# Kernel tuning notes

Hardware: AMD Instinct MI355X
Metric: run time of the kernel (lower is better)

## Reference

```python
import jax, jax.numpy as jnp
import numpy as np

BETA = 0.25
NUM_CODES = 512      # K
CODE_DIM = 64        # D (codebook_size)
N_TOKENS = 131072    # N


def setup_inputs() -> dict:
    key = jax.random.key(0)
    kx, kc = jax.random.split(key)
    x = jax.random.normal(kx, (N_TOKENS, CODE_DIM), dtype=jnp.float32)
    # keras 'random_uniform' initializer: U(-0.05, 0.05)
    codebook = jax.random.uniform(kc, (NUM_CODES, CODE_DIM), dtype=jnp.float32,
                                  minval=-0.05, maxval=0.05)
    return {"x": x, "codebook": codebook}


def reference(x, codebook):
    # Squared Euclidean distances [N, K] via expansion; argmin is identical
    # to argmin of tf.norm (sqrt is monotone).
    x2 = jnp.sum(x * x, axis=-1, keepdims=True)            # [N, 1]
    c2 = jnp.sum(codebook * codebook, axis=-1)             # [K]
    d2 = x2 - 2.0 * (x @ codebook.T) + c2[None, :]         # [N, K]
    indices = jnp.argmin(d2, axis=-1)                      # [N]
    quantized = jnp.take(codebook, indices, axis=0)        # [N, D]

    commitment_loss = jnp.mean((jax.lax.stop_gradient(quantized) - x) ** 2)
    codebook_loss = jnp.mean((quantized - jax.lax.stop_gradient(x)) ** 2)
    loss = BETA * commitment_loss + codebook_loss

    # straight-through estimator
    quantized_st = x + jax.lax.stop_gradient(quantized - x)
    return quantized_st, loss
```

## Files before the change

kernel.cpp:

```cpp
#include <hip/hip_runtime.h>

#define N_TOK 131072
#define K_CODES 512
#define DIM 64
#define MARGIN_S 1e-4f
#define LIST_CAP 30000

typedef __attribute__((ext_vector_type(8))) short bfx8;
typedef __attribute__((ext_vector_type(4))) float f32x4;
typedef __attribute__((ext_vector_type(4))) int i32x4;

__device__ __forceinline__ unsigned short f2bf_rn(float f) {
    unsigned u = __float_as_uint(f);
    unsigned r = (u + 0x7FFF + ((u >> 16) & 1)) >> 16;
    return (unsigned short)r;
}
__device__ __forceinline__ float bf2f(unsigned short h) {
    return __uint_as_float(((unsigned)h) << 16);
}

__device__ __forceinline__ float np_sumsq64(const float* v) {
    float r[8];
#pragma unroll
    for (int j = 0; j < 8; ++j) r[j] = __fmul_rn(v[j], v[j]);
#pragma unroll
    for (int i = 8; i < 64; i += 8) {
#pragma unroll
        for (int j = 0; j < 8; ++j)
            r[j] = __fadd_rn(r[j], __fmul_rn(v[i + j], v[i + j]));
    }
    return __fadd_rn(__fadd_rn(__fadd_rn(r[0], r[1]), __fadd_rn(r[2], r[3])),
                     __fadd_rn(__fadd_rn(r[4], r[5]), __fadd_rn(r[6], r[7])));
}

__global__ __launch_bounds__(256) void vq_prep(
    const float* __restrict__ cb, float* __restrict__ cnorm,
    float* __restrict__ c2h, unsigned short* __restrict__ cbh,
    unsigned short* __restrict__ cbl)
{
    int k = blockIdx.x * 256 + threadIdx.x;
    if (k >= K_CODES) return;
    float v[DIM];
#pragma unroll
    for (int d = 0; d < DIM; ++d) {
        float f = cb[k * DIM + d];
        v[d] = f;
        unsigned short h = f2bf_rn(f);
        cbh[k * DIM + d] = h;
        cbl[k * DIM + d] = f2bf_rn(__fsub_rn(f, bf2f(h)));
    }
    float c2 = np_sumsq64(v);
    cnorm[k] = c2;
    c2h[k] = __fmul_rn(0.5f, c2);
}

__global__ __attribute__((amdgpu_flat_work_group_size(256, 256),
                          amdgpu_waves_per_eu(2, 2)))
void vq_screen(
    const float* __restrict__ x, const float* __restrict__ cb,
    const unsigned short* __restrict__ cbh, const unsigned short* __restrict__ cbl,
    const float* __restrict__ c2h, float* __restrict__ out,
    double* __restrict__ loss_acc, int* __restrict__ counter,
    int* __restrict__ list, int cap)
{
    __shared__ bfx8 lds_h[128 * 8];
    __shared__ bfx8 lds_l[128 * 8];
    __shared__ float lds_c2[K_CODES];
    __shared__ double wsum[4];

    const int tid = threadIdx.x;
    const int wave = (blockIdx.x << 2) + (tid >> 6);
    const int lane = tid & 63;
    const int tokb = wave << 6;
    const int lrow = lane & 15;
    const int lgrp = lane >> 4;
    const int lcol = lrow;

    const float inf = __int_as_float(0x7f800000);

    if (tid < 128) ((float4*)lds_c2)[tid] = ((const float4*)c2h)[tid];

#define SPL(F, J, AH, AL) { unsigned short h_ = f2bf_rn(F); \
    (AH)[J] = (short)h_; (AL)[J] = (short)f2bf_rn(__fsub_rn(F, bf2f(h_))); }
#define LOADX(m) \
    bfx8 ah0_##m, al0_##m, ah1_##m, al1_##m; \
    { const float* xr = x + ((size_t)(tokb + (m) * 16 + lrow) << 6) + (lgrp << 3); \
      float4 f0 = *(const float4*)xr; \
      float4 f1 = *(const float4*)(xr + 4); \
      float4 f2 = *(const float4*)(xr + 32); \
      float4 f3 = *(const float4*)(xr + 36); \
      SPL(f0.x, 0, ah0_##m, al0_##m) SPL(f0.y, 1, ah0_##m, al0_##m) \
      SPL(f0.z, 2, ah0_##m, al0_##m) SPL(f0.w, 3, ah0_##m, al0_##m) \
      SPL(f1.x, 4, ah0_##m, al0_##m) SPL(f1.y, 5, ah0_##m, al0_##m) \
      SPL(f1.z, 6, ah0_##m, al0_##m) SPL(f1.w, 7, ah0_##m, al0_##m) \
      SPL(f2.x, 0, ah1_##m, al1_##m) SPL(f2.y, 1, ah1_##m, al1_##m) \
      SPL(f2.z, 2, ah1_##m, al1_##m) SPL(f2.w, 3, ah1_##m, al1_##m) \
      SPL(f3.x, 4, ah1_##m, al1_##m) SPL(f3.y, 5, ah1_##m, al1_##m) \
      SPL(f3.z, 6, ah1_##m, al1_##m) SPL(f3.w, 7, ah1_##m, al1_##m) }
    LOADX(0) LOADX(1) LOADX(2) LOADX(3)
#undef LOADX
#undef SPL

    f32x4 best0 = {inf, inf, inf, inf}, best1 = best0, best2 = best0, best3 = best0;
    f32x4 sec0 = best0, sec1 = best0, sec2 = best0, sec3 = best0;
    i32x4 idx0 = {0, 0, 0, 0}, idx1 = idx0, idx2 = idx0, idx3 = idx0;

    for (int ph = 0; ph < 4; ++ph) {
        __syncthreads();
        {
            const bfx8* gh = (const bfx8*)cbh + (ph << 10);
            const bfx8* gl = (const bfx8*)cbl + (ph << 10);
#pragma unroll
            for (int it = 0; it < 4; ++it) {
                int g = (it << 8) + tid;
                int code = g >> 3, slot = g & 7;
                int dst = (code << 3) + (slot ^ (code & 7));
                lds_h[dst] = gh[g];
                lds_l[dst] = gl[g];
            }
        }
        __syncthreads();

        int lr_c = lrow;
        int s0_c = lgrp ^ (lr_c & 7);
        bfx8 bh0 = lds_h[(lr_c << 3) + s0_c];
        bfx8 bh1 = lds_h[(lr_c << 3) + (s0_c ^ 4)];
        bfx8 bl0 = lds_l[(lr_c << 3) + s0_c];
        bfx8 bl1 = lds_l[(lr_c << 3) + (s0_c ^ 4)];
        float cn = lds_c2[(ph << 7) + lr_c];

#pragma unroll
        for (int ctl = 0; ctl < 8; ++ctl) {
            const int code = (ph << 7) + (ctl << 4) + lrow;
            bfx8 nh0 = bh0, nh1 = bh1, nl0 = bl0, nl1 = bl1;
            float cnn = cn;
            if (ctl < 7) {
                int lr_n = ((ctl + 1) << 4) + lrow;
                int s0_n = lgrp ^ (lr_n & 7);
                nh0 = lds_h[(lr_n << 3) + s0_n];
                nh1 = lds_h[(lr_n << 3) + (s0_n ^ 4)];
                nl0 = lds_l[(lr_n << 3) + s0_n];
                nl1 = lds_l[(lr_n << 3) + (s0_n ^ 4)];
                cnn = lds_c2[(ph << 7) + lr_n];
            }

#define MACC(m) \
            f32x4 accP##m = {0.f, 0.f, 0.f, 0.f}; \
            f32x4 accQ##m = {0.f, 0.f, 0.f, 0.f}; \
            accP##m = __builtin_amdgcn_mfma_f32_16x16x32_bf16(ah0_##m, bh0, accP##m, 0, 0, 0); \
            accQ##m = __builtin_amdgcn_mfma_f32_16x16x32_bf16(ah1_##m, bh1, accQ##m, 0, 0, 0); \
            accP##m = __builtin_amdgcn_mfma_f32_16x16x32_bf16(al0_##m, bh0, accP##m, 0, 0, 0); \
            accQ##m = __builtin_amdgcn_mfma_f32_16x16x32_bf16(al1_##m, bh1, accQ##m, 0, 0, 0); \
            accP##m = __builtin_amdgcn_mfma_f32_16x16x32_bf16(ah0_##m, bl0, accP##m, 0, 0, 0); \
            accQ##m = __builtin_amdgcn_mfma_f32_16x16x32_bf16(ah1_##m, bl1, accQ##m, 0, 0, 0);
            MACC(0) MACC(1) MACC(2) MACC(3)
#undef MACC

#define UPD1(m, R) { float s = cn - (accP##m[R] + accQ##m[R]); \
            bool p = s < best##m[R]; \
            sec##m[R] = p ? best##m[R] : fminf(sec##m[R], s); \
            best##m[R] = p ? s : best##m[R]; \
            idx##m[R] = p ? code : idx##m[R]; }
#define UPDM(m) UPD1(m, 0) UPD1(m, 1) UPD1(m, 2) UPD1(m, 3)
            UPDM(0) UPDM(1) UPDM(2) UPDM(3)
#undef UPDM
#undef UPD1

            bh0 = nh0; bh1 = nh1; bl0 = nl0; bl1 = nl1; cn = cnn;
        }
    }

    i32x4 pk0, pk1, pk2, pk3;
#define REDR(m, R) { float b = best##m[R], sc = sec##m[R]; int ix = idx##m[R]; \
    _Pragma("unroll") \
    for (int off = 1; off < 16; off <<= 1) { \
        float ob = __shfl_xor(b, off, 64); \
        float os = __shfl_xor(sc, off, 64); \
        int   oi = __shfl_xor(ix, off, 64); \
        bool take = (ob < b) || (ob == b && oi < ix); \
        float ns = take ? fminf(b, os) : fminf(sc, ob); \
        b = take ? ob : b; ix = take ? oi : ix; sc = ns; } \
    pk##m[R] = ix | (((sc - b) < MARGIN_S) ? (1 << 30) : 0); }
#define REDM(m) REDR(m, 0) REDR(m, 1) REDR(m, 2) REDR(m, 3)
    REDM(0) REDM(1) REDM(2) REDM(3)
#undef REDM
#undef REDR

    double ls = 0.0;
#define EPI1(m, R) { int fi = pk##m[R]; \
    int bidx_t = fi & 0xFFFF; \
    int t = tokb + (m) * 16 + (lgrp << 2) + (R); \
    float4 xv = *((const float4*)(x + ((size_t)t << 6)) + lcol); \
    float4 qv = *((const float4*)(cb + ((size_t)bidx_t << 6)) + lcol); \
    float4 ov; \
    float e0 = __fsub_rn(qv.x, xv.x); ov.x = __fadd_rn(xv.x, e0); \
    float e1 = __fsub_rn(qv.y, xv.y); ov.y = __fadd_rn(xv.y, e1); \
    float e2 = __fsub_rn(qv.z, xv.z); ov.z = __fadd_rn(xv.z, e2); \
    float e3 = __fsub_rn(qv.w, xv.w); ov.w = __fadd_rn(xv.w, e3); \
    *((float4*)(out + ((size_t)t << 6)) + lcol) = ov; \
    if (!(fi >> 30)) \
        ls += (double)e0 * e0 + (double)e1 * e1 + (double)e2 * e2 + (double)e3 * e3; \
    else if (lcol == 0) { int pos = atomicAdd(counter, 1); \
                          if (pos < cap) list[pos] = t; } }
#define EPIM(m) EPI1(m, 0) EPI1(m, 1) EPI1(m, 2) EPI1(m, 3)
    EPIM(0) EPIM(1) EPIM(2) EPIM(3)
#undef EPIM
#undef EPI1

#pragma unroll
    for (int off = 32; off > 0; off >>= 1) ls += __shfl_down(ls, off, 64);
    if (lane == 0) wsum[tid >> 6] = ls;
    __syncthreads();
    if (tid == 0)
        atomicAdd(loss_acc, (wsum[0] + wsum[1]) + (wsum[2] + wsum[3]));
}

__global__ __launch_bounds__(256) void vq_rerank(
    const float* __restrict__ x, const float* __restrict__ cb,
    const float* __restrict__ cnorm, float* __restrict__ out,
    double* __restrict__ loss_acc, const int* __restrict__ counter,
    const int* __restrict__ list, int cap)
{
    int cnt = *counter; if (cnt > cap) cnt = cap;
    const int lane = threadIdx.x & 63;
    const int wid = (blockIdx.x << 2) + (threadIdx.x >> 6);
    const int nw = gridDim.x << 2;
    double ls = 0.0;

    for (int i = wid; i < cnt; i += nw) {
        const int t = list[i];
        float xr[DIM];
        {
            const float4* xv = (const float4*)(x + ((size_t)t << 6));
#pragma unroll
            for (int q = 0; q < 16; ++q) {
                float4 v = xv[q];
                xr[4 * q + 0] = v.x; xr[4 * q + 1] = v.y;
                xr[4 * q + 2] = v.z; xr[4 * q + 3] = v.w;
            }
        }
        const float x2 = np_sumsq64(xr);
        float best = __int_as_float(0x7f800000);
        int bi = 0;
#pragma unroll 2
        for (int j = 0; j < 8; ++j) {
            const int k = (j << 6) + lane;
            const float4* c = (const float4*)(cb + ((size_t)k << 6));
            float a = 0.f;
#pragma unroll
            for (int q = 0; q < 16; ++q) {
                float4 f = c[q];
                a = __fmaf_rn(xr[4 * q + 0], f.x, a);
                a = __fmaf_rn(xr[4 * q + 1], f.y, a);
                a = __fmaf_rn(xr[4 * q + 2], f.z, a);
                a = __fmaf_rn(xr[4 * q + 3], f.w, a);
            }
            float d2 = __fadd_rn(__fsub_rn(x2, __fmul_rn(2.0f, a)), cnorm[k]);
            bool p = d2 < best;
            best = p ? d2 : best; bi = p ? k : bi;
        }
#pragma unroll
        for (int off = 1; off < 64; off <<= 1) {
            float ob = __shfl_xor(best, off, 64);
            int   oi = __shfl_xor(bi, off, 64);
            bool take = (ob < best) || (ob == best && oi < bi);
            best = take ? ob : best; bi = take ? oi : bi;
        }
        float xv = x[((size_t)t << 6) + lane];
        float q  = cb[((size_t)bi << 6) + lane];
        float e = __fsub_rn(q, xv);
        out[((size_t)t << 6) + lane] = __fadd_rn(xv, e);
        ls += (double)e * (double)e;
    }
#pragma unroll
    for (int off = 32; off > 0; off >>= 1) ls += __shfl_down(ls, off, 64);
    if (lane == 0 && ls != 0.0) atomicAdd(loss_acc, ls);
}

__global__ void vq_final(const double* __restrict__ loss_acc,
                         float* __restrict__ out_loss)
{
    if (threadIdx.x == 0 && blockIdx.x == 0) {
        double mean = *loss_acc / (double)((size_t)N_TOK * DIM);
        *out_loss = (float)(1.25 * mean);
    }
}

extern "C" void kernel_launch(void* const* d_in, const int* in_sizes, int n_in,
                              void* d_out, int out_size, void* d_ws, size_t ws_size,
                              hipStream_t stream) {
    const float* x  = (const float*)d_in[0];
    const float* cb = (const float*)d_in[1];
    float* out = (float*)d_out;
    float* out_loss = out + (size_t)N_TOK * DIM;

    char* ws = (char*)d_ws;
    double* loss_acc = (double*)ws;
    int* counter = (int*)(ws + 8);
    float* cnorm = (float*)(ws + 64);
    float* c2h = (float*)(ws + 2112);
    unsigned short* cbh = (unsigned short*)(ws + 4608);
    unsigned short* cbl = (unsigned short*)(ws + 70144);
    int* list = (int*)(ws + 135680);

    hipMemsetAsync(d_ws, 0, 16, stream);
    vq_prep<<<2, 256, 0, stream>>>(cb, cnorm, c2h, cbh, cbl);
    vq_screen<<<N_TOK / 256, 256, 0, stream>>>(x, cb, cbh, cbl, c2h, out,
                                               loss_acc, counter, list, LIST_CAP);
    vq_rerank<<<256, 256, 0, stream>>>(x, cb, cnorm, out, loss_acc,
                                       counter, list, LIST_CAP);
    vq_final<<<1, 64, 0, stream>>>(loss_acc, out_loss);
}
```

Before: 84.71 us.

## Fold code norm into MFMA accumulator, simplify argmin update, fuse final loss

The screening pass now seeds the MFMA accumulator with the negated half code norm, which drops the per-element subtraction, and rewrites the best/second-best update with fmin/fmax in place of selects. The screening margin is halved so fewer tokens go to the exact rerank pass. The final loss kernel is removed: the last rerank block, found through an atomic done counter, computes the mean. vq_prep also runs as 8 blocks of 64 threads instead of 2 of 256. The smaller margin risks missing near-ties, and the last-block pattern relies on threadfence ordering.

```diff
diff --git a/kernel.cpp b/kernel.cpp
--- a/kernel.cpp
+++ b/kernel.cpp
@@ -3,7 +3,7 @@
 #define N_TOK 131072
 #define K_CODES 512
 #define DIM 64
-#define MARGIN_S 1e-4f
+#define MARGIN_S 5e-5f
 #define LIST_CAP 30000
 
 typedef __attribute__((ext_vector_type(8))) short bfx8;
@@ -33,12 +33,12 @@
                      __fadd_rn(__fadd_rn(r[4], r[5]), __fadd_rn(r[6], r[7])));
 }
 
-__global__ __launch_bounds__(256) void vq_prep(
+__global__ __launch_bounds__(64) void vq_prep(
     const float* __restrict__ cb, float* __restrict__ cnorm,
     float* __restrict__ c2h, unsigned short* __restrict__ cbh,
     unsigned short* __restrict__ cbl)
 {
-    int k = blockIdx.x * 256 + threadIdx.x;
+    int k = blockIdx.x * 64 + threadIdx.x;
     if (k >= K_CODES) return;
     float v[DIM];
 #pragma unroll
@@ -51,7 +51,7 @@
     }
     float c2 = np_sumsq64(v);
     cnorm[k] = c2;
-    c2h[k] = __fmul_rn(0.5f, c2);
+    c2h[k] = __fmul_rn(-0.5f, c2);
 }
 
 __global__ __attribute__((amdgpu_flat_work_group_size(256, 256),
@@ -127,13 +127,13 @@
         bfx8 bh1 = lds_h[(lr_c << 3) + (s0_c ^ 4)];
         bfx8 bl0 = lds_l[(lr_c << 3) + s0_c];
         bfx8 bl1 = lds_l[(lr_c << 3) + (s0_c ^ 4)];
-        float cn = lds_c2[(ph << 7) + lr_c];
+        float nc = lds_c2[(ph << 7) + lr_c];
 
 #pragma unroll
         for (int ctl = 0; ctl < 8; ++ctl) {
             const int code = (ph << 7) + (ctl << 4) + lrow;
             bfx8 nh0 = bh0, nh1 = bh1, nl0 = bl0, nl1 = bl1;
-            float cnn = cn;
+            float ncn = nc;
             if (ctl < 7) {
                 int lr_n = ((ctl + 1) << 4) + lrow;
                 int s0_n = lgrp ^ (lr_n & 7);
@@ -141,11 +141,11 @@
                 nh1 = lds_h[(lr_n << 3) + (s0_n ^ 4)];
                 nl0 = lds_l[(lr_n << 3) + s0_n];
                 nl1 = lds_l[(lr_n << 3) + (s0_n ^ 4)];
-                cnn = lds_c2[(ph << 7) + lr_n];
+                ncn = lds_c2[(ph << 7) + lr_n];
             }
 
 #define MACC(m) \
-            f32x4 accP##m = {0.f, 0.f, 0.f, 0.f}; \
+            f32x4 accP##m = {nc, nc, nc, nc}; \
             f32x4 accQ##m = {0.f, 0.f, 0.f, 0.f}; \
             accP##m = __builtin_amdgcn_mfma_f32_16x16x32_bf16(ah0_##m, bh0, accP##m, 0, 0, 0); \
             accQ##m = __builtin_amdgcn_mfma_f32_16x16x32_bf16(ah1_##m, bh1, accQ##m, 0, 0, 0); \
@@ -156,17 +156,18 @@
             MACC(0) MACC(1) MACC(2) MACC(3)
 #undef MACC
 
-#define UPD1(m, R) { float s = cn - (accP##m[R] + accQ##m[R]); \
+#define UPD1(m, R) { float s = -(accP##m[R] + accQ##m[R]); \
+            float mx = fmaxf(s, best##m[R]); \
+            sec##m[R] = fminf(sec##m[R], mx); \
             bool p = s < best##m[R]; \
-            sec##m[R] = p ? best##m[R] : fminf(sec##m[R], s); \
-            best##m[R] = p ? s : best##m[R]; \
+            best##m[R] = fminf(best##m[R], s); \
             idx##m[R] = p ? code : idx##m[R]; }
 #define UPDM(m) UPD1(m, 0) UPD1(m, 1) UPD1(m, 2) UPD1(m, 3)
             UPDM(0) UPDM(1) UPDM(2) UPDM(3)
 #undef UPDM
 #undef UPD1
 
-            bh0 = nh0; bh1 = nh1; bl0 = nl0; bl1 = nl1; cn = cnn;
+            bh0 = nh0; bh1 = nh1; bl0 = nl0; bl1 = nl1; nc = ncn;
         }
     }
 
@@ -215,16 +216,18 @@
         atomicAdd(loss_acc, (wsum[0] + wsum[1]) + (wsum[2] + wsum[3]));
 }
 
+#define RERANK_BLOCKS 256
 __global__ __launch_bounds__(256) void vq_rerank(
     const float* __restrict__ x, const float* __restrict__ cb,
     const float* __restrict__ cnorm, float* __restrict__ out,
     double* __restrict__ loss_acc, const int* __restrict__ counter,
-    const int* __restrict__ list, int cap)
+    const int* __restrict__ list, int cap,
+    int* __restrict__ done, float* __restrict__ out_loss)
 {
     int cnt = *counter; if (cnt > cap) cnt = cap;
     const int lane = threadIdx.x & 63;
     const int wid = (blockIdx.x << 2) + (threadIdx.x >> 6);
-    const int nw = gridDim.x << 2;
+    const int nw = RERANK_BLOCKS << 2;
     double ls = 0.0;
 
     for (int i = wid; i < cnt; i += nw) {
@@ -274,15 +277,20 @@
     }
 #pragma unroll
     for (int off = 32; off > 0; off >>= 1) ls += __shfl_down(ls, off, 64);
-    if (lane == 0 && ls != 0.0) atomicAdd(loss_acc, ls);
-}
-
-__global__ void vq_final(const double* __restrict__ loss_acc,
-                         float* __restrict__ out_loss)
-{
-    if (threadIdx.x == 0 && blockIdx.x == 0) {
-        double mean = *loss_acc / (double)((size_t)N_TOK * DIM);
-        *out_loss = (float)(1.25 * mean);
+    __shared__ double wsum[4];
+    if (lane == 0) wsum[threadIdx.x >> 6] = ls;
+    __syncthreads();
+    if (threadIdx.x == 0) {
+        double tot = (wsum[0] + wsum[1]) + (wsum[2] + wsum[3]);
+        if (tot != 0.0) atomicAdd(loss_acc, tot);
+        __threadfence();
+        int prev = atomicAdd(done, 1);
+        if (prev == RERANK_BLOCKS - 1) {
+            __threadfence();
+            double total = atomicAdd(loss_acc, 0.0);
+            double mean = total / (double)((size_t)N_TOK * DIM);
+            *out_loss = (float)(1.25 * mean);
+        }
     }
 }
 
@@ -297,17 +305,18 @@
     char* ws = (char*)d_ws;
     double* loss_acc = (double*)ws;
     int* counter = (int*)(ws + 8);
+    int* done = (int*)(ws + 12);
     float* cnorm = (float*)(ws + 64);
     float* c2h = (float*)(ws + 2112);
     unsigned short* cbh = (unsigned short*)(ws + 4608);
     unsigned short* cbl = (unsigned short*)(ws + 70144);
     int* list = (int*)(ws + 135680);
 
-    hipMemsetAsync(d_ws, 0, 16, stream);
-    vq_prep<<<2, 256, 0, stream>>>(cb, cnorm, c2h, cbh, cbl);
+    hipMemsetAsync(d_ws, 0, 32, stream);
+    vq_prep<<<8, 64, 0, stream>>>(cb, cnorm, c2h, cbh, cbl);
     vq_screen<<<N_TOK / 256, 256, 0, stream>>>(x, cb, cbh, cbl, c2h, out,
                                                loss_acc, counter, list, LIST_CAP);
-    vq_rerank<<<256, 256, 0, stream>>>(x, cb, cnorm, out, loss_acc,
-                                       counter, list, LIST_CAP);
-    vq_final<<<1, 64, 0, stream>>>(loss_acc, out_loss);
-}
+    vq_rerank<<<RERANK_BLOCKS, 256, 0, stream>>>(x, cb, cnorm, out, loss_acc,
+                                                 counter, list, LIST_CAP,
+                                                 done, out_loss);
+}
```

After: 211.9 us. +150.1%, slower.
